# Performance work log

Measured on AMD Instinct MI355X. Metric: run time of the kernel, lower is better.

Reference implementation:

```python
import jax, jax.numpy as jnp
import numpy as np

B, S, D, H = 2, 2048, 1024, 16
HD = D // H                      # head_dim = 64
F_POLY = HD + HD * HD            # 4160 degree-2 poly feature dim
M_HID = 2 * D                    # memory_expansion = 2
FFN_H = int(D * 4 * 2 / 3)       # 2730 SwiGLU hidden
GG_H = 64                        # gamma-gate hidden dim
EPS = 1e-6
OMEGA_W, OMEGA_DECAY = 64, 0.95
TTL_ALPHA, TTL_ETA, NS_ITERS = 0.999, 0.01, 5


def rmsnorm(x, w):
    return x * jax.lax.rsqrt(jnp.mean(x * x, -1, keepdims=True) + EPS) * w


def apply_rope(q, k):
    half = HD // 2
    inv = 1.0 / (10000.0 ** (jnp.arange(half, dtype=jnp.float32) / half))
    fr = jnp.arange(S, dtype=jnp.float32)[:, None] * inv[None, :]  # (S, half)
    cos, sin = jnp.cos(fr), jnp.sin(fr)
    def rot(x):
        x1, x2 = x[..., :half], x[..., half:]
        return jnp.concatenate([x1 * cos - x2 * sin, x1 * sin + x2 * cos], -1)
    return rot(q), rot(k)


def phi2(z):
    # degree-2 polynomial features: [z, vec(z z^T)/sqrt(d)]  -> capacity O(d_k^2)
    outer = (z[..., :, None] * z[..., None, :]).reshape(*z.shape[:-1], HD * HD)
    return jnp.concatenate([z, outer / jnp.sqrt(jnp.float32(HD))], -1)


def memory_forward(x, wk, w1, w2):
    feat = phi2(x @ wk)                     # (B,S,F_POLY)
    return jax.nn.silu(feat @ w1) @ w2      # (B,S,D)


def newton_schulz(G):
    # Muon-style quintic Newton-Schulz orthogonalization
    a, b, c = 3.4445, -4.7750, 2.0315
    X = G / (jnp.linalg.norm(G) + 1e-7)
    tall = X.shape[0] > X.shape[1]
    X = X.T if tall else X
    for _ in range(NS_ITERS):
        A = X @ X.T
        X = a * X + (b * A + c * (A @ A)) @ X
    return X.T if tall else X


def block_forward(x, norm1_w, norm2_w, qkv_w, q_norm_w, k_norm_w,
                  gamma_w1, gamma_w2, mem_wk, mem_w1, mem_w2,
                  memory_gate, wo_w, ffn_w1, ffn_w2, ffn_w3):
    h = rmsnorm(x, norm1_w)
    q, k, v = jnp.split(h @ qkv_w, 3, axis=-1)
    heads = lambda t: t.reshape(B, S, H, HD).transpose(0, 2, 1, 3)  # (B,H,S,HD)
    q, k, v = heads(q), heads(k), heads(v)
    q = rmsnorm(q, q_norm_w)   # qk-norm per head
    k = rmsnorm(k, k_norm_w)
    q, k = apply_rope(q, k)

    # input-dependent gamma gate (B,S,1)
    gamma = jax.nn.sigmoid(jax.nn.silu(h @ gamma_w1) @ gamma_w2)

    # causal QK memory projection: gamma-blended causal mean of keys
    k_cummean = jnp.cumsum(k, axis=2) / jnp.arange(1, S + 1, dtype=k.dtype)[None, None, :, None]
    g = gamma[:, None, :, :]                          # (B,1,S,1)
    q_mem = g * q + (1.0 - g) * k_cummean             # (B,H,S,HD)
    q_mem_flat = q_mem.transpose(0, 2, 1, 3).reshape(B, S, D)
    v_flat = v.transpose(0, 2, 1, 3).reshape(B, S, D)

    # --- TTL: Omega-rule loss + Newton-Schulz update of memory params ---
    pos = jnp.arange(S)
    dpow = jnp.float32(OMEGA_DECAY) ** (S - 1 - pos).astype(jnp.float32)
    dpow = jnp.where(pos >= S - OMEGA_W, dpow, 0.0)   # context-window pruning
    w_omega = gamma[..., 0] * dpow                    # (B,S)

    def omega_loss(wk, w1, w2):
        pred = memory_forward(q_mem_flat, wk, w1, w2)
        per_tok = jnp.sum((pred - v_flat) ** 2, -1)   # (B,S)
        return jnp.sum(w_omega * per_tok) / (jnp.sum(w_omega) + 1e-8)

    gk, g1, g2 = jax.grad(omega_loss, argnums=(0, 1, 2))(mem_wk, mem_w1, mem_w2)
    # momentum S_t = theta*0 + grad (fresh state), update M = alpha*M - eta*NS(S_t)
    mem_wk_u = TTL_ALPHA * mem_wk - TTL_ETA * newton_schulz(gk)
    mem_w1_u = TTL_ALPHA * mem_w1 - TTL_ETA * newton_schulz(g1)
    mem_w2_u = TTL_ALPHA * mem_w2 - TTL_ETA * newton_schulz(g2)

    # --- SWA branch (full causal attention) ---
    attn = jnp.einsum('bhsd,bhtd->bhst', q, k) * (HD ** -0.5)
    causal = jnp.tril(jnp.ones((S, S), dtype=bool))
    attn = jnp.where(causal, attn, -jnp.inf)
    attn = jax.nn.softmax(attn, -1)
    attn_out = jnp.einsum('bhst,bhtd->bhsd', attn, v)
    attn_out = attn_out.transpose(0, 2, 1, 3).reshape(B, S, D) @ wo_w

    # --- memory branch with learned output-level gate ---
    mem_out = memory_forward(q_mem_flat, mem_wk_u, mem_w1_u, mem_w2_u)
    mem_out = jax.nn.sigmoid(memory_gate) * mem_out

    x = x + attn_out + mem_out
    h2 = rmsnorm(x, norm2_w)
    x = x + (jax.nn.silu(h2 @ ffn_w1) * (h2 @ ffn_w3)) @ ffn_w2
    return x


def setup_inputs() -> dict:
    key = jax.random.key(0)
    ks = jax.random.split(key, 16)
    std = 0.02
    return {
        'x': jax.random.normal(ks[0], (B, S, D), jnp.float32),
        'norm1_w': jnp.ones((D,), jnp.float32),
        'norm2_w': jnp.ones((D,), jnp.float32),
        'qkv_w': jax.random.normal(ks[1], (D, 3 * D), jnp.float32) * std,
        'q_norm_w': jnp.ones((HD,), jnp.float32),
        'k_norm_w': jnp.ones((HD,), jnp.float32),
        'gamma_w1': jax.random.normal(ks[2], (D, GG_H), jnp.float32) * std,
        'gamma_w2': jnp.zeros((GG_H, 1), jnp.float32),  # zero-init -> gamma ~ 0.5
        'mem_wk': jax.random.normal(ks[3], (D, HD), jnp.float32) * std,
        'mem_w1': jax.random.normal(ks[4], (F_POLY, M_HID), jnp.float32) * std,
        'mem_w2': jax.random.normal(ks[5], (M_HID, D), jnp.float32) * std,
        'memory_gate': jnp.zeros((1,), jnp.float32),    # layer 0 -> pre-sigmoid 0.0
        'wo_w': jax.random.normal(ks[6], (D, D), jnp.float32) * (std / 2 ** 0.5),
        'ffn_w1': jax.random.normal(ks[7], (D, FFN_H), jnp.float32) * std,
        'ffn_w2': jax.random.normal(ks[8], (FFN_H, D), jnp.float32) * std,
        'ffn_w3': jax.random.normal(ks[9], (D, FFN_H), jnp.float32) * std,
    }


def reference(x, norm1_w, norm2_w, qkv_w, q_norm_w, k_norm_w, gamma_w1, gamma_w2,
              mem_wk, mem_w1, mem_w2, memory_gate, wo_w, ffn_w1, ffn_w2, ffn_w3):
    return block_forward(x, norm1_w, norm2_w, qkv_w, q_norm_w, k_norm_w,
                         gamma_w1, gamma_w2, mem_wk, mem_w1, mem_w2,
                         memory_gate, wo_w, ffn_w1, ffn_w2, ffn_w3)
```

## Files before the change

### kernel.cpp

```cpp
#include <hip/hip_runtime.h>
#include <math.h>

#define Bc 2
#define Sc 2048
#define Dc 1024
#define Hc 16
#define HDc 64
#define FPOLY 4160
#define MHID 2048
#define FFNH 2730
#define FFNHP 2752
#define GGH 64
#define NTOK 4096
#define NACT 128

typedef __bf16 bf16;
typedef __attribute__((ext_vector_type(8))) __bf16 bf16x8;
typedef __attribute__((ext_vector_type(4))) float f32x4;

#define AS1 __attribute__((address_space(1)))
#define AS3 __attribute__((address_space(3)))

__device__ __forceinline__ void gload16(const void* g, void* l) {
    __builtin_amdgcn_global_load_lds((AS1 const void*)g, (AS3 void*)l, 16, 0, 0);
// ... 493 lines not shown
__global__ __launch_bounds__(256) void ns_fused(
    const bf16* __restrict__ Sg, const bf16* __restrict__ Cg,
    bf16* __restrict__ Fcg, bf16* __restrict__ FcTg)
{
    __shared__ bf16 Cl[16384], Ml[16384], MTl[16384], FTl[16384];
    const int z = blockIdx.x;
    const bf16* S = Sg + (size_t)z * 16384;
    bf16* Fc = Fcg + (size_t)z * 16384;
    bf16* FcT = FcTg + (size_t)z * 16384;
    const int tid = threadIdx.x, w = tid >> 6, lane = tid & 63;
    const int lrow = lane & 15, quad = lane >> 4;
    const int bm = w * 32;
    for (int i = tid; i < 2048; i += 256) {
        const int row = i >> 4, c = i & 15;
        *(bf16x8*)&Cl[row * 128 + ((c ^ (row & 7)) << 3)] =
            *(const bf16x8*)(Cg + (size_t)z * 16384 + (size_t)row * 128 + c * 8);
    }
    __syncthreads();
    const int r0 = bm + lrow, r1 = r0 + 16;
    const int rx = lrow & 7;
    f32x4 acc[2][8];
    auto zacc = [&]() {
#pragma unroll
        for (int mt = 0; mt < 2; ++mt)
#pragma unroll
            for (int nt = 0; nt < 8; ++nt) { acc[mt][nt][0] = 0.f; acc[mt][nt][1] = 0.f; acc[mt][nt][2] = 0.f; acc[mt][nt][3] = 0.f; }
    };
    auto inner = [&](bf16x8 af0, bf16x8 af1, const bf16* Bt, int c) {
#pragma unroll
        for (int nt = 0; nt < 8; ++nt) {
            const int br = nt * 16 + lrow;
            bf16x8 bfr = *(const bf16x8*)&Bt[br * 128 + ((c ^ (br & 7)) << 3)];
            acc[0][nt] = __builtin_amdgcn_mfma_f32_16x16x32_bf16(af0, bfr, acc[0][nt], 0, 0, 0);
            acc[1][nt] = __builtin_amdgcn_mfma_f32_16x16x32_bf16(af1, bfr, acc[1][nt], 0, 0, 0);
        }
    };
    auto gemm_ll = [&](const bf16* Al, const bf16* Bt) {
        zacc();
#pragma unroll
        for (int k0 = 0; k0 < 128; k0 += 32) {
            const int c = (k0 >> 3) + quad;
            bf16x8 af0 = *(const bf16x8*)&Al[r0 * 128 + ((c ^ rx) << 3)];
            bf16x8 af1 = *(const bf16x8*)&Al[r1 * 128 + ((c ^ rx) << 3)];
            inner(af0, af1, Bt, c);
        }
    };
    auto gemm_gl = [&](const bf16* Ag, const bf16* Bt) {
        zacc();
#pragma unroll
        for (int k0 = 0; k0 < 128; k0 += 32) {
            const int c = (k0 >> 3) + quad;
            bf16x8 af0 = *(const bf16x8*)(Ag + (size_t)r0 * 128 + k0 + quad * 8);
            bf16x8 af1 = *(const bf16x8*)(Ag + (size_t)r1 * 128 + k0 + quad * 8);
            inner(af0, af1, Bt, c);
        }
    };

    for (int t = 0; t < 5; ++t) {
        gemm_gl(S, Cl);
#pragma unroll
        for (int mt = 0; mt < 2; ++mt)
#pragma unroll
            for (int nt = 0; nt < 8; ++nt)
#pragma unroll
                for (int r = 0; r < 4; ++r) {
                    const int row = bm + mt * 16 + quad * 4 + r, col = nt * 16 + lrow;
                    const bf16 v = (bf16)acc[mt][nt][r];
                    Ml[swz(row, col)] = v;
                    MTl[swz(col, row)] = v;
                }
        __syncthreads();
        gemm_ll(Ml, MTl);
#pragma unroll
        for (int mt = 0; mt < 2; ++mt)
#pragma unroll
            for (int nt = 0; nt < 8; ++nt)
#pragma unroll
                for (int r = 0; r < 4; ++r) {
                    const int row = bm + mt * 16 + quad * 4 + r, col = nt * 16 + lrow;
                    float v = 2.0315f * acc[mt][nt][r] - 4.775f * (float)Ml[swz(row, col)];
                    if (row == col) v += 3.4445f;
                    FTl[swz(col, row)] = (bf16)v;
                    if (t == 0) Fc[(size_t)row * 128 + col] = (bf16)v;
                }
        __syncthreads();
        if (t > 0) {
            gemm_gl(Fc, FTl);
            if (t == 4) {
#pragma unroll
                for (int mt = 0; mt < 2; ++mt)
#pragma unroll
                    for (int nt = 0; nt < 8; ++nt)
#pragma unroll
                        for (int r = 0; r < 4; ++r) {
                            const int row = bm + mt * 16 + quad * 4 + r, col = nt * 16 + lrow;
                            FcT[(size_t)col * 128 + row] = (bf16)acc[mt][nt][r];
                        }
                return;
            }
#pragma unroll
            for (int mt = 0; mt < 2; ++mt)
#pragma unroll
                for (int nt = 0; nt < 8; ++nt)
#pragma unroll
                    for (int r = 0; r < 4; ++r) {
                        const int row = bm + mt * 16 + quad * 4 + r, col = nt * 16 + lrow;
                        Fc[(size_t)row * 128 + col] = (bf16)acc[mt][nt][r];
                    }
        }
        gemm_ll(Cl, FTl);
#pragma unroll
        for (int mt = 0; mt < 2; ++mt)
#pragma unroll
            for (int nt = 0; nt < 8; ++nt)
#pragma unroll
                for (int r = 0; r < 4; ++r) {
                    const int row = bm + mt * 16 + quad * 4 + r, col = nt * 16 + lrow;
                    Ml[swz(col, row)] = (bf16)acc[mt][nt][r];
                }
        __syncthreads();
        gemm_ll(Ml, FTl);
#pragma unroll
        for (int mt = 0; mt < 2; ++mt)
#pragma unroll
            for (int nt = 0; nt < 8; ++nt)
#pragma unroll
                for (int r = 0; r < 4; ++r) {
                    const int row = bm + mt * 16 + quad * 4 + r, col = nt * 16 + lrow;
                    Cl[swz(row, col)] = (bf16)acc[mt][nt][r];
                }
        __syncthreads();
    }
}

__global__ __launch_bounds__(256) void tconv_kernel(
    const float* __restrict__ W, bf16* __restrict__ Wt, int K, int N, int Kpad,
    bf16* __restrict__ Wc)
{
    __shared__ float t[32][33];
    const int k0 = blockIdx.x * 32, n0 = blockIdx.y * 32;
    const int tx = threadIdx.x & 31, ty = threadIdx.x >> 5;
#pragma unroll
    for (int r = 0; r < 4; ++r) {
        int gk = k0 + ty + r * 8, gn = n0 + tx;
        bool ok = (gk < K && gn < N);
        float v = ok ? W[(size_t)gk * N + gn] : 0.f;
        t[ty + r * 8][tx] = v;
        if (Wc && ok) Wc[(size_t)gk * N + gn] = (bf16)v;
    }
    __syncthreads();
#pragma unroll
    for (int r = 0; r < 4; ++r) {
        int gn = n0 + ty + r * 8, gk = k0 + tx;
        if (gn < N && gk < Kpad) Wt[(size_t)gn * Kpad + gk] = (bf16)t[tx][ty + r * 8];
    }
}

__global__ __launch_bounds__(256) void tconv6_kernel(
    const float* __restrict__ s0, const float* __restrict__ s1,
    const float* __restrict__ s2, const float* __restrict__ s3,
    const float* __restrict__ s4, const float* __restrict__ s5,
    bf16* __restrict__ d0, bf16* __restrict__ d1, bf16* __restrict__ d2,
    bf16* __restrict__ d3, bf16* __restrict__ d4, bf16* __restrict__ d5)
{
    const int zz = blockIdx.z;
    const float* W; bf16* Wt; int N;
    if      (zz == 0) { W = s0; Wt = d0; N = 2048; }
    else if (zz == 1) { W = s1; Wt = d1; N = 1024; }
    else if (zz == 2) { W = s2; Wt = d2; N = 64;   }
    else if (zz == 3) { W = s3; Wt = d3; N = 1024; }
    else if (zz == 4) { W = s4; Wt = d4; N = 4160; }
    else              { W = s5; Wt = d5; N = 2048; }
    const int k0 = blockIdx.x * 32, n0 = blockIdx.y * 32;
    if (n0 >= N) return;
    __shared__ float t[32][33];
    const int tx = threadIdx.x & 31, ty = threadIdx.x >> 5;
#pragma unroll
    for (int r = 0; r < 4; ++r) {
        int gk = k0 + ty + r * 8, gn = n0 + tx;
        t[ty + r * 8][tx] = (gk < 128 && gn < N) ? W[(size_t)gk * N + gn] : 0.f;
    }
    __syncthreads();
#pragma unroll
    for (int r = 0; r < 4; ++r) {
        int gn = n0 + ty + r * 8, gk = k0 + tx;
        if (gn < N) Wt[(size_t)gn * 128 + gk] = (bf16)t[tx][ty + r * 8];
    }
}

__global__ __launch_bounds__(256) void vtrans_kernel(
    const bf16* __restrict__ qkv, bf16* __restrict__ vt)
{
    __shared__ bf16 t[32][33];
    const int s0 = blockIdx.x * 32, d0 = blockIdx.y * 32, bh = blockIdx.z;
    const int b = bh >> 4, h = bh & 15;
    const int tx = threadIdx.x & 31, ty = threadIdx.x >> 5;
#pragma unroll
    for (int r = 0; r < 4; ++r) {
        int s = s0 + ty + r * 8;
        t[ty + r * 8][tx] = qkv[((size_t)b * Sc + s) * 3072 + 2048 + h * 64 + d0 + tx];
    }
    __syncthreads();
#pragma unroll
    for (int r = 0; r < 4; ++r) {
        int d = d0 + ty + r * 8;
        vt[((size_t)bh * 64 + d) * Sc + s0 + tx] = t[tx][ty + r * 8];
    }
}

__global__ __launch_bounds__(256) void rms_rows(
    const float* __restrict__ in, const float* __restrict__ w,
    bf16* __restrict__ out, int D)
{
    const int row = blockIdx.x;
    const float* r = in + (size_t)row * D;
    bf16* o = out + (size_t)row * D;
    float s = 0.f;
    for (int i = threadIdx.x; i < D; i += 256) { float v = r[i]; s += v * v; }
    __shared__ float red[256];
    red[threadIdx.x] = s;
    __syncthreads();
    for (int st = 128; st; st >>= 1) {
        if (threadIdx.x < st) red[threadIdx.x] += red[threadIdx.x + st];
        __syncthreads();
    }
    float rs = rsqrtf(red[0] / (float)D + 1e-6f);
    for (int i = threadIdx.x; i < D; i += 256) o[i] = (bf16)(r[i] * rs * w[i]);
}

__global__ __launch_bounds__(256) void gamma_kernel(
    const float* __restrict__ gg1, const float* __restrict__ w2,
    float* __restrict__ gamma)
{
    const int tid = threadIdx.x, w = tid >> 6, lane = tid & 63;
    const int t = blockIdx.x * 4 + w;
    float v = gg1[(size_t)t * GGH + lane];
    v = v / (1.f + expf(-v));
    v *= w2[lane];
#pragma unroll
    for (int off = 32; off; off >>= 1) v += __shfl_xor(v, off);
    if (lane == 0) gamma[t] = 1.f / (1.f + expf(-v));
}

__global__ __launch_bounds__(256) void snr_qk(
    const bf16* __restrict__ src, const float* __restrict__ qw, const float* __restrict__ kw,
    bf16* __restrict__ qd, bf16* __restrict__ kd)
{
    const int tid = threadIdx.x, wv = tid >> 6, lane = tid & 63;
    const int s = blockIdx.x * 4 + wv;
    const int y = blockIdx.y, b = blockIdx.z;
    const int h = y & 15, which = y >> 4;
    const float* w = which ? kw : qw;
    bf16* dst = which ? kd : qd;
    const size_t row = ((size_t)b * Sc + s) * 3072 + which * 1024 + h * 64;
    float v = (float)src[row + lane];
    float ss = v * v;
#pragma unroll
    for (int off = 32; off; off >>= 1) ss += __shfl_xor(ss, off);
    v = v * rsqrtf(ss / 64.f + 1e-6f) * w[lane];
    const int j = lane & 31;
    float inv = powf(10000.f, -(float)j / 32.f);
    float ang = (float)s * inv;
    float sn = sinf(ang), cs = cosf(ang);
    float p = __shfl_xor(v, 32);
    float o;
    if (lane < 32) o = v * cs - p * sn;
    else           o = p * sn + v * cs;
    const size_t od = (((size_t)b * Hc + h) * Sc + s) * 64 + lane;
    dst[od] = (bf16)o;
}

__global__ void kpsum_kernel(const bf16* __restrict__ kn, float* __restrict__ psum)
{
    const int bh = blockIdx.x, c = blockIdx.y, d = threadIdx.x;
    const size_t base = (size_t)bh * Sc * 64 + (size_t)c * 128 * 64 + d;
    float s = 0.f;
    for (int i = 0; i < 128; ++i) s += (float)kn[base + (size_t)i * 64];
    psum[((size_t)bh * 16 + c) * 64 + d] = s;
}

__global__ void qmem2_kernel(
    const bf16* __restrict__ qn, const bf16* __restrict__ kn,
    const float* __restrict__ gamma, const float* __restrict__ psum,
    float* __restrict__ qmem, bf16* __restrict__ qmemb)
{
    const int bh = blockIdx.x, c = blockIdx.y;
    const int b = bh >> 4, hh = bh & 15;
    const int d = threadIdx.x;
    const size_t base = (size_t)bh * Sc * 64;
    float run = 0.f;
    for (int cc = 0; cc < c; ++cc) run += psum[((size_t)bh * 16 + cc) * 64 + d];
    for (int s = c * 128; s < c * 128 + 128; ++s) {
        run += (float)kn[base + (size_t)s * 64 + d];
        float cm = run / (float)(s + 1);
        float g = gamma[b * Sc + s];
        float qv = (float)qn[base + (size_t)s * 64 + d];
        float val = g * qv + (1.f - g) * cm;
        const size_t o = ((size_t)(b * Sc + s)) * Dc + hh * 64 + d;
        qmem[o] = val;
        qmemb[o] = (bf16)val;
    }
}

__global__ __launch_bounds__(256, 4) void attn_mfma(
    const bf16* __restrict__ qn, const bf16* __restrict__ kn,
    const bf16* __restrict__ vt, bf16* __restrict__ outp)
{
    const int flat = blockIdx.x;
    const int glow = flat & 7, t2 = flat >> 3;
    const int xq = t2 & 31, ghigh = t2 >> 5;
    const int g = glow | (ghigh << 3);
    const int h = g & 15, b = g >> 4;
    const int bh = b * Hc + h;
    const int tid = threadIdx.x, w = tid >> 6, lane = tid & 63;
    const int lrow = lane & 15, quad = lane >> 4;
    const int rhalf = w & 1, pgrp = w >> 1;
    __shared__ bf16 Ps[4][16][136];
    __shared__ float Ob[2][16][68];
    __shared__ float Lb[2][16];
    const bf16* kbase = kn + (size_t)bh * Sc * 64;
    const bf16* vtb = vt + (size_t)bh * 64 * Sc;
    const float SC = 0.1803368801f;
#pragma unroll 1
    for (int ti = 0; ti < 2; ++ti) {
        const int zt = ti ? (63 - xq) : xq;
        const int qb = zt * 32;
        const int nc = (qb >> 7) + 1;
        const int par = pgrp ^ ti;
        const int rowg = qb + rhalf * 16 + quad * 4;
        bf16x8 qf[2];
        const bf16* qbase = qn + ((size_t)bh * Sc + qb + rhalf * 16) * 64;
#pragma unroll
        for (int ks = 0; ks < 2; ++ks)
            qf[ks] = *(const bf16x8*)(qbase + (size_t)lrow * 64 + ks * 32 + quad * 8);
        f32x4 oacc[4];
#pragma unroll
        for (int nt = 0; nt < 4; ++nt) { oacc[nt][0] = 0.f; oacc[nt][1] = 0.f; oacc[nt][2] = 0.f; oacc[nt][3] = 0.f; }
        float lsum[4] = {0.f, 0.f, 0.f, 0.f};
        for (int ci = par; ci < nc; ci += 2) {
            const int k0 = ci << 7;
            f32x4 sacc[8];
#pragma unroll
            for (int nt = 0; nt < 8; ++nt) { sacc[nt][0] = 0.f; sacc[nt][1] = 0.f; sacc[nt][2] = 0.f; sacc[nt][3] = 0.f; }
            __builtin_amdgcn_s_setprio(1);
#pragma unroll
            for (int ks = 0; ks < 2; ++ks) {
#pragma unroll
                for (int nh = 0; nh < 2; ++nh) {
                    bf16x8 kf[4];
#pragma unroll
                    for (int j = 0; j < 4; ++j)
                        kf[j] = *(const bf16x8*)(kbase + (size_t)(k0 + (nh * 4 + j) * 16 + lrow) * 64 + ks * 32 + quad * 8);
#pragma unroll
                    for (int j = 0; j < 4; ++j)
                        sacc[nh * 4 + j] = __builtin_amdgcn_mfma_f32_16x16x32_bf16(qf[ks], kf[j], sacc[nh * 4 + j], 0, 0, 0);
                }
            }
            __builtin_amdgcn_s_setprio(0);
#pragma unroll
            for (int nt = 0; nt < 8; ++nt) {
                const int kc = k0 + nt * 16 + lrow;
#pragma unroll
                for (int r = 0; r < 4; ++r) {
                    float p = (kc > rowg + r) ? 0.f : fexp2(fmaf(sacc[nt][r], SC, -12.f));
                    sacc[nt][r] = p;
                    lsum[r] += p;
                }
            }
#pragma unroll
            for (int nt = 0; nt < 8; ++nt)
#pragma unroll
                for (int r = 0; r < 4; ++r)
                    Ps[w][quad * 4 + r][nt * 16 + lrow] = (bf16)sacc[nt][r];
            __builtin_amdgcn_s_setprio(1);
#pragma unroll
            for (int ks2 = 0; ks2 < 4; ++ks2) {
                bf16x8 pf = *(const bf16x8*)&Ps[w][lrow][ks2 * 32 + quad * 8];
#pragma unroll
                for (int nt = 0; nt < 4; ++nt) {
                    bf16x8 vf = *(const bf16x8*)(vtb + (size_t)(nt * 16 + lrow) * Sc + k0 + ks2 * 32 + quad * 8);
                    oacc[nt] = __builtin_amdgcn_mfma_f32_16x16x32_bf16(pf, vf, oacc[nt], 0, 0, 0);
                }
            }
            __builtin_amdgcn_s_setprio(0);
        }
#pragma unroll
        for (int r = 0; r < 4; ++r)
#pragma unroll
            for (int off = 1; off < 16; off <<= 1) lsum[r] += __shfl_xor(lsum[r], off);
        if (pgrp == 1) {
#pragma unroll
            for (int nt = 0; nt < 4; ++nt)
#pragma unroll
                for (int r = 0; r < 4; ++r)
                    Ob[rhalf][quad * 4 + r][nt * 16 + lrow] = oacc[nt][r];
            if (lrow == 0)
#pragma unroll
                for (int r = 0; r < 4; ++r) Lb[rhalf][quad * 4 + r] = lsum[r];
        }
        __syncthreads();
        if (pgrp == 0) {
            float linv[4];
#pragma unroll
            for (int r = 0; r < 4; ++r)
                linv[r] = 1.f / (lsum[r] + Lb[rhalf][quad * 4 + r]);
#pragma unroll
            for (int nt = 0; nt < 4; ++nt)
#pragma unroll
                for (int r = 0; r < 4; ++r) {
                    const float o2 = Ob[rhalf][quad * 4 + r][nt * 16 + lrow];
                    outp[((size_t)b * Sc + rowg + r) * Dc + h * 64 + nt * 16 + lrow] =
                        (bf16)((oacc[nt][r] + o2) * linv[r]);
                }
        }
        __syncthreads();
    }
}

__global__ __launch_bounds__(256) void gather_active(
    const float* __restrict__ qmem, const bf16* __restrict__ qkv,
    float* __restrict__ xa, bf16* __restrict__ xab, float* __restrict__ va)
{
    const int t = blockIdx.x;
    const int b = t >> 6;
    const int s = Sc - 64 + (t & 63);
    const float* qrow = qmem + ((size_t)(b * Sc + s)) * Dc;
    const bf16* vrow = qkv + ((size_t)(b * Sc + s)) * 3072 + 2048;
    for (int i = threadIdx.x; i < Dc; i += 256) {
        float q = qrow[i];
        xa[(size_t)t * Dc + i] = q;
        xab[(size_t)t * Dc + i] = (bf16)q;
        va[(size_t)t * Dc + i] = (float)vrow[i];
    }
}

__global__ void wvec_kernel(const float* __restrict__ gamma,
                            float* __restrict__ wvec, float* __restrict__ wsum)
{
    const int t = threadIdx.x;
    const int b = t >> 6, si = t & 63;
    const int s = Sc - 64 + si;
    float v = gamma[b * Sc + s] * powf(0.95f, (float)(Sc - 1 - s));
    wvec[t] = v;
    __shared__ float red[128];
    red[t] = v; __syncthreads();
    for (int st = 64; st; st >>= 1) { if (t < st) red[t] += red[t + st]; __syncthreads(); }
    if (t == 0) wsum[0] = red[0];
}

__global__ __launch_bounds__(256) void phi2_f32(
    const float* __restrict__ z, float* __restrict__ feat, bf16* __restrict__ featb)
{
    const int f = blockIdx.x * 256 + threadIdx.x;
    const int t = blockIdx.y;
    if (f >= FPOLY) return;
    const float* zr = z + (size_t)t * 64;
    float v;
    if (f < 64) v = zr[f];
    else { int i = (f - 64) >> 6, j = (f - 64) & 63; v = zr[i] * zr[j] * 0.125f; }
    feat[(size_t)t * FPOLY + f] = v;
    featb[(size_t)t * FPOLY + f] = (bf16)v;
}

__global__ __launch_bounds__(256) void phi2_bf16(
    const float* __restrict__ z, bf16* __restrict__ feat)
{
    const int f = blockIdx.x * 256 + threadIdx.x;
    const int t = blockIdx.y;
    if (f >= FPOLY) return;
    const float* zr = z + (size_t)t * 64;
    float v;
    if (f < 64) v = zr[f];
    else { int i = (f - 64) >> 6, j = (f - 64) & 63; v = zr[i] * zr[j] * 0.125f; }
    feat[(size_t)t * FPOLY + f] = (bf16)v;
}

__global__ void dz_kernel(const float* __restrict__ dfeat, const float* __restrict__ za,
                          float* __restrict__ dz, bf16* __restrict__ dzb)
{
    const int t = blockIdx.x;
    const int k = threadIdx.x;
    const float* df = dfeat + (size_t)t * FPOLY;
    const float* z = za + (size_t)t * 64;
    float s1 = 0.f, s2 = 0.f;
    for (int j = 0; j < 64; ++j) {
        float zj = z[j];
        s1 += df[64 + k * 64 + j] * zj;
        s2 += df[64 + j * 64 + k] * zj;
    }
    float v = df[k] + 0.125f * (s1 + s2);
    dz[(size_t)t * 64 + k] = v;
    dzb[(size_t)t * 64 + k] = (bf16)v;
}

__global__ void sgate_kernel(const float* __restrict__ mg, float* __restrict__ out)
{
    out[0] = 1.f / (1.f + expf(-mg[0]));
}

__global__ void swiglu_pack(const bf16* __restrict__ u, bf16* __restrict__ o)
{
    int i = blockIdx.x * 256 + threadIdx.x;
    if (i >= NTOK * FFNHP) return;
    int t = i / FFNHP, k = i % FFNHP;
    if (k >= FFNH) { o[i] = (bf16)0.f; return; }
    float a = (float)u[(size_t)t * 5504 + k];
    float b = (float)u[(size_t)t * 5504 + 2752 + k];
    o[i] = (bf16)(a / (1.f + __expf(-a)) * b);
}

extern "C" void kernel_launch(void* const* d_in, const int* in_sizes, int n_in,
                              void* d_out, int out_size, void* d_ws, size_t ws_size,
                              hipStream_t stream)
{
    const float* x     = (const float*)d_in[0];
    const float* n1w   = (const float*)d_in[1];
    const float* n2w   = (const float*)d_in[2];
    const float* qkvw  = (const float*)d_in[3];
    const float* qnw   = (const float*)d_in[4];
    const float* knw   = (const float*)d_in[5];
    const float* gw1   = (const float*)d_in[6];
    const float* gw2   = (const float*)d_in[7];
    const float* mwk   = (const float*)d_in[8];
    const float* mw1   = (const float*)d_in[9];
    const float* mw2   = (const float*)d_in[10];
    const float* mgate = (const float*)d_in[11];
    const float* wow   = (const float*)d_in[12];
    const float* fw1   = (const float*)d_in[13];
    const float* fw2   = (const float*)d_in[14];
    const float* fw3   = (const float*)d_in[15];
    float* outp = (float*)d_out;

    char* base = (char*)d_ws;
    size_t off = 0;
    auto takeB = [&](size_t bytes) { char* p = base + off; off += (bytes + 255) & ~(size_t)255; return p; };

    char* slabA  = takeB(22544384);
    char* slabE  = takeB(22544384);
    char* slabBC = takeB(16777216);
    char* slabD  = takeB(8388608);
    char* slabF  = takeB(8388608);
    char* slabG  = takeB(17301504);
    float* partA = (float*)slabA;
    bf16* vt     = (bf16*)slabA;
    bf16* featC4 = (bf16*)slabA;
    bf16* ff13b  = (bf16*)slabA;
    float* qmem  = (float*)slabE;
    bf16* qnb = (bf16*)slabBC;    bf16* knb = (bf16*)(slabBC + 8388608);
    float* x2 = (float*)slabBC;
    bf16* qmemb = (bf16*)slabD;
    bf16* t1b4  = (bf16*)slabD;
    bf16* attnb = (bf16*)slabF;
    bf16* hb = (bf16*)slabG;      bf16* mw1b = (bf16*)slabG;
    bf16* w1uT = (bf16*)slabG;    bf16* h2b = (bf16*)slabG;
    bf16* qkvb = (bf16*)takeB(25165824);
    bf16* ffpk = qkvb;

    bf16* qkvwT = (bf16*)takeB(6291456);
    bf16* gw1T  = (bf16*)takeB(262144);
    bf16* wowT  = (bf16*)takeB(2097152);
    bf16* mw1T  = (bf16*)takeB(17039360);
    bf16* mw2T  = (bf16*)takeB(4194304);
    bf16* fw13T = (bf16*)takeB(11272192);
    bf16* fw2T  = (bf16*)takeB(5636096);
    bf16* mw2b  = (bf16*)takeB(4194304);
    bf16* mwkTb = (bf16*)takeB(262144);
    bf16* wkuTb = (bf16*)takeB(262144);
    bf16* w2uT  = (bf16*)takeB(4194304);

    float* zf    = (float*)takeB(1048576);
    float* gg1   = (float*)takeB(1048576);
    float* gamma = (float*)takeB(16384);
    float* wvec  = (float*)takeB(512);
    float* scal  = (float*)takeB(256);
    float* psum  = (float*)takeB(131072);
    float* xa    = (float*)takeB(524288);
    float* va    = (float*)takeB(524288);
    float* za    = (float*)takeB(32768);
    float* featA = (float*)takeB(2129920);
    float* ua    = (float*)takeB(1048576);
    float* sua   = (float*)takeB(1048576);
    float* dpreda= (float*)takeB(524288);
    float* dua   = (float*)takeB(1048576);
    float* dfeata= (float*)takeB(2129920);
    float* dza   = (float*)takeB(32768);
    float* SA    = (float*)takeB(196608);
    float* CA    = (float*)takeB(196608);
    bf16* featAb = (bf16*)takeB(1064960);
    bf16* suab   = (bf16*)takeB(524288);
    bf16* xab    = (bf16*)takeB(262144);
    bf16* duab   = (bf16*)takeB(524288);
    bf16* dpredab= (bf16*)takeB(262144);
    bf16* dzab   = (bf16*)takeB(16384);
    bf16* PT1Tb  = (bf16*)takeB(524288);
    bf16* PT2Tb  = (bf16*)takeB(262144);
    bf16* PT3Tb  = (bf16*)takeB(32768);
    bf16* duaTb  = (bf16*)takeB(524288);
    bf16* dpredaTb=(bf16*)takeB(262144);
    bf16* dzaTb  = (bf16*)takeB(32768);
    bf16* xaTb   = (bf16*)takeB(262144);
    bf16* featATb= (bf16*)takeB(1081344);
    bf16* suaTb  = (bf16*)takeB(524288);
    bf16* Sb16  = (bf16*)takeB(98304);
    bf16* Cb16  = (bf16*)takeB(98304);
    bf16* FcAb  = (bf16*)takeB(98304);
    bf16* FcTAb = (bf16*)takeB(98304);

    auto gemmB = [&](int outbf, int cinbf, const bf16* A, const bf16* Bt,
                     const void* Cin, void* C, int M, int N, int K, int ldc,
                     float alpha, float beta, int act, const float* sptr) {
        dim3 grid((N + 127) / 128, M / 128);
        if (outbf && cinbf) gemm_bt<1, 1><<<grid, 256, 0, stream>>>(A, Bt, Cin, C, M, N, K, ldc, alpha, beta, act, sptr);
        else if (outbf)     gemm_bt<1, 0><<<grid, 256, 0, stream>>>(A, Bt, Cin, C, M, N, K, ldc, alpha, beta, act, sptr);
        else                gemm_bt<0, 0><<<grid, 256, 0, stream>>>(A, Bt, Cin, C, M, N, K, ldc, alpha, beta, act, sptr);
    };
    auto gemm64 = [&](const bf16* A, const bf16* Bt, const float* Cin, float* C,
                      int M, int N, int K, int ldc, const float* sptr) {
        dim3 grid(N / 64, M / 128);
        gemm_bt64<<<grid, 256, 0, stream>>>(A, Bt, Cin, C, M, N, K, ldc, sptr);
    };
    auto gdir = [&](int outbf, int cinbf, const bf16* A, const bf16* Bt,
                    const void* Cin, void* C, int M, int N, int K, int ldc,
                    float alpha, float beta, int act, const float* sptr) {
        dim3 grid((N + 127) / 128, (M + 127) / 128);
        if (outbf && cinbf)      gemm_direct<1, 1><<<grid, 256, 0, stream>>>(A, Bt, Cin, C, M, N, K, ldc, alpha, beta, act, sptr);
        else if (outbf)          gemm_direct<1, 0><<<grid, 256, 0, stream>>>(A, Bt, Cin, C, M, N, K, ldc, alpha, beta, act, sptr);
        else if (cinbf)          gemm_direct<0, 1><<<grid, 256, 0, stream>>>(A, Bt, Cin, C, M, N, K, ldc, alpha, beta, act, sptr);
        else                     gemm_direct<0, 0><<<grid, 256, 0, stream>>>(A, Bt, Cin, C, M, N, K, ldc, alpha, beta, act, sptr);
    };
    auto skp = [&](const bf16* A, const bf16* Bt, float* out,
                   int M, int N, int K, int KC) {
        int SK = (K + KC - 1) / KC;
        gemm_skp<<<dim3((N + 127) / 128, (M + 127) / 128, SK), 256, 0, stream>>>(A, Bt, partA, M, N, K, KC);
        int MN = M * N;
        skred<<<(MN + 255) / 256, 256, 0, stream>>>(partA, out, SK, MN);
    };
    auto tconv = [&](const float* W, bf16* Wt, int K, int N, int Kpad, bf16* Wc) {
        tconv_kernel<<<dim3((Kpad + 31) / 32, (N + 31) / 32), 256, 0, stream>>>(W, Wt, K, N, Kpad, Wc);
    };

    tconv(qkvw, qkvwT, Dc, 3 * Dc, Dc, nullptr);
    tconv(gw1, gw1T, Dc, GGH, Dc, nullptr);
    tconv(wow, wowT, Dc, Dc, Dc, nullptr);
    tconv(mw2, mw2T, MHID, Dc, MHID, mw2b);
    tconv(fw1, fw13T, Dc, FFNH, Dc, nullptr);
    tconv(fw3, fw13T + (size_t)2752 * Dc, Dc, FFNH, Dc, nullptr);
    tconv(fw2, fw2T, FFNH, Dc, FFNHP, nullptr);
    tconv(mwk, mwkTb, Dc, HDc, Dc, nullptr);
    sgate_kernel<<<1, 1, 0, stream>>>(mgate, scal + 2);

    rms_rows<<<NTOK, 256, 0, stream>>>(x, n1w, hb, Dc);
    gemmB(1, 0, hb, qkvwT, nullptr, qkvb, NTOK, 3 * Dc, Dc, 3 * Dc, 1.f, 0.f, 0, nullptr);
    snr_qk<<<dim3(Sc / 4, 32, Bc), 256, 0, stream>>>(qkvb, qnw, knw, qnb, knb);
    skp(hb, gw1T, gg1, NTOK, GGH, Dc, 256);
    gamma_kernel<<<NTOK / 4, 256, 0, stream>>>(gg1, gw2, gamma);
    tconv(mw1, mw1T, FPOLY, MHID, FPOLY, mw1b);

    vtrans_kernel<<<dim3(Sc / 32, 2, Bc * Hc), 256, 0, stream>>>(qkvb, vt);
    kpsum_kernel<<<dim3(Bc * Hc, 16), 64, 0, stream>>>(knb, psum);
    qmem2_kernel<<<dim3(Bc * Hc, 16), 64, 0, stream>>>(qnb, knb, gamma, psum, qmem, qmemb);
    attn_mfma<<<dim3(1024), 256, 0, stream>>>(qnb, knb, vt, attnb);

    gather_active<<<NACT, 256, 0, stream>>>(qmem, qkvb, xa, xab, va);
    wvec_kernel<<<1, 128, 0, stream>>>(gamma, wvec, scal);

    skp(xab, mwkTb, za, NACT, HDc, Dc, 64);
    phi2_f32<<<dim3((FPOLY + 255) / 256, NACT), 256, 0, stream>>>(za, featA, featAb);
    gemm_skp<<<dim3(16, 1, 15), 256, 0, stream>>>(featAb, mw1T, partA, NACT, MHID, FPOLY, 288);
    skred_silu<<<1024, 256, 0, stream>>>(partA, ua, sua, suab);
    gemm_skp<<<dim3(8, 1, 16), 256, 0, stream>>>(suab, mw2T, partA, NACT, Dc, MHID, 128);
    skred_dpred<<<512, 256, 0, stream>>>(partA, va, wvec, scal, dpreda, dpredab);
    gemm_skp<<<dim3(16, 1, 8), 256, 0, stream>>>(dpredab, mw2b, partA, NACT, MHID, Dc, 128);
    skred_dsilu<<<1024, 256, 0, stream>>>(partA, ua, dua, duab);
    skp(duab, mw1b, dfeata, NACT, FPOLY, MHID, 256);
    dz_kernel<<<NACT, 64, 0, stream>>>(dfeata, za, dza, dzab);

    tconv6_kernel<<<dim3(4, 130, 6), 256, 0, stream>>>(
        dua, dpreda, dza, xa, featA, sua,
        duaTb, dpredaTb, dzaTb, xaTb, featATb, suaTb);

    gram_trick<<<1, 256, 0, stream>>>(za, SA);
    gram_bat<<<dim3(32, 5), 256, 0, stream>>>(suab, xab, duab, dpredab, dzab, partA);
    gram_red<<<320, 256, 0, stream>>>(partA, SA, CA);
    ns_norm_kernel<<<3, 256, 0, stream>>>(SA, CA, Sb16, Cb16, scal + 8);
    ns_fused<<<3, 256, 0, stream>>>(Sb16, Cb16, FcAb, FcTAb);
    gdir3_kernel<<<dim3(1, 16, 3), 256, 0, stream>>>(
        duaTb, dpredaTb, dzaTb, FcTAb, PT1Tb, PT2Tb, PT3Tb, scal + 8);

    gdir(1, 1, PT3Tb, xaTb, mwkTb, wkuTb, HDc, Dc, 128, Dc, -0.01f, 0.999f, 0, nullptr);
    gemmB(1, 1, PT1Tb, featATb, mw1T, w1uT, MHID, FPOLY, 128, FPOLY, -0.01f, 0.999f, 0, nullptr);
    gemmB(1, 1, PT2Tb, suaTb, mw2T, w2uT, Dc, MHID, 128, MHID, -0.01f, 0.999f, 0, nullptr);

    gemm64(attnb, wowT, x, x2, NTOK, Dc, Dc, Dc, nullptr);
    skp(qmemb, wkuTb, zf, NTOK, HDc, Dc, 128);

    phi2_bf16<<<dim3((FPOLY + 255) / 256, NTOK), 256, 0, stream>>>(zf, featC4);
    gemmB(1, 0, featC4, w1uT, nullptr, t1b4, NTOK, MHID, FPOLY, MHID, 1.f, 0.f, 1, nullptr);
    gemm64(t1b4, w2uT, x2, x2, NTOK, Dc, MHID, Dc, scal + 2);

    rms_rows<<<NTOK, 256, 0, stream>>>(x2, n2w, h2b, Dc);
    gemmB(1, 0, h2b, fw13T, nullptr, ff13b, NTOK, 5482, Dc, 5504, 1.f, 0.f, 0, nullptr);
    swiglu_pack<<<(NTOK * FFNHP + 255) / 256, 256, 0, stream>>>(ff13b, ffpk);
    gemm64(ffpk, fw2T, x2, outp, NTOK, Dc, FFNHP, Dc, nullptr);
}
```

Baseline: 1.162 ms.

## Stage K/V tiles in double-buffered LDS and widen attention query tiles

The causal attention kernel now stages each 128-key K and V^T tile into XOR-swizzled shared memory with async global-to-LDS loads. The tiles are double-buffered so the next tile loads while the current one is computed. Each block handles two 64-row query tiles, paired for causal balance, and every wave owns 16 rows over the full key range, which removes the cross-wave partial-sum merge. The grid is halved and the occupancy hint is dropped, so there is less parallelism and higher LDS use per block in exchange for removing redundant global K/V reads by each wave.

```diff
diff --git a/kernel.cpp b/kernel.cpp
--- a/kernel.cpp
+++ b/kernel.cpp
@@ -819,119 +819,140 @@
     }
 }
 
-__global__ __launch_bounds__(256, 4) void attn_mfma(
+__global__ __launch_bounds__(256) void attn_mfma(
     const bf16* __restrict__ qn, const bf16* __restrict__ kn,
     const bf16* __restrict__ vt, bf16* __restrict__ outp)
 {
     const int flat = blockIdx.x;
     const int glow = flat & 7, t2 = flat >> 3;
-    const int xq = t2 & 31, ghigh = t2 >> 5;
+    const int p = t2 & 15, ghigh = t2 >> 4;
     const int g = glow | (ghigh << 3);
     const int h = g & 15, b = g >> 4;
     const int bh = b * Hc + h;
     const int tid = threadIdx.x, w = tid >> 6, lane = tid & 63;
     const int lrow = lane & 15, quad = lane >> 4;
-    const int rhalf = w & 1, pgrp = w >> 1;
-    __shared__ bf16 Ps[4][16][136];
-    __shared__ float Ob[2][16][68];
-    __shared__ float Lb[2][16];
+    __shared__ bf16 Ks[2][128 * 64];
+    __shared__ bf16 Vs[2][64 * 128];
+    __shared__ bf16 Ps[4][16][72];
     const bf16* kbase = kn + (size_t)bh * Sc * 64;
     const bf16* vtb = vt + (size_t)bh * 64 * Sc;
     const float SC = 0.1803368801f;
-#pragma unroll 1
-    for (int ti = 0; ti < 2; ++ti) {
-        const int zt = ti ? (63 - xq) : xq;
-        const int qb = zt * 32;
-        const int nc = (qb >> 7) + 1;
-        const int par = pgrp ^ ti;
-        const int rowg = qb + rhalf * 16 + quad * 4;
-        bf16x8 qf[2];
-        const bf16* qbase = qn + ((size_t)bh * Sc + qb + rhalf * 16) * 64;
+    const int zt0 = p, zt1 = 31 - p;
+    const int nc0 = (zt0 >> 1) + 1, nc1 = (zt1 >> 1) + 1;
+    const int nct = nc0 + nc1;
+    const int krr = lane >> 3, kur = lane & 7;
+    const int vrr = lane >> 4, vur = lane & 15;
+    auto stage = [&](int bi, int k0) {
+#pragma unroll
+        for (int rr = 0; rr < 4; ++rr) {
+            const int row = (rr * 4 + w) * 8 + krr;
+            gload16(kbase + (size_t)(k0 + row) * 64 + ((kur ^ krr) << 3),
+                    (char*)&Ks[bi][0] + (rr * 4 + w) * 1024);
+        }
+#pragma unroll
+        for (int rr = 0; rr < 4; ++rr) {
+            const int vrow = (rr * 4 + w) * 4 + vrr;
+            gload16(vtb + (size_t)vrow * Sc + k0 + ((vur ^ (vrow & 7)) << 3),
+                    (char*)&Vs[bi][0] + (rr * 4 + w) * 1024);
+        }
+    };
+    int qb = zt0 * 64;
+    int rowg = qb + w * 16 + quad * 4;
+    bf16x8 qf[2];
+    {
+        const bf16* qbase = qn + ((size_t)bh * Sc + qb + w * 16) * 64;
 #pragma unroll
         for (int ks = 0; ks < 2; ++ks)
             qf[ks] = *(const bf16x8*)(qbase + (size_t)lrow * 64 + ks * 32 + quad * 8);
-        f32x4 oacc[4];
-#pragma unroll
-        for (int nt = 0; nt < 4; ++nt) { oacc[nt][0] = 0.f; oacc[nt][1] = 0.f; oacc[nt][2] = 0.f; oacc[nt][3] = 0.f; }
-        float lsum[4] = {0.f, 0.f, 0.f, 0.f};
-        for (int ci = par; ci < nc; ci += 2) {
-            const int k0 = ci << 7;
-            f32x4 sacc[8];
-#pragma unroll
-            for (int nt = 0; nt < 8; ++nt) { sacc[nt][0] = 0.f; sacc[nt][1] = 0.f; sacc[nt][2] = 0.f; sacc[nt][3] = 0.f; }
+    }
+    f32x4 oacc[4];
+#pragma unroll
+    for (int nt = 0; nt < 4; ++nt) { oacc[nt][0] = 0.f; oacc[nt][1] = 0.f; oacc[nt][2] = 0.f; oacc[nt][3] = 0.f; }
+    float lsum[4] = {0.f, 0.f, 0.f, 0.f};
+    auto writeout = [&]() {
+#pragma unroll
+        for (int r = 0; r < 4; ++r)
+#pragma unroll
+            for (int off = 1; off < 16; off <<= 1) lsum[r] += __shfl_xor(lsum[r], off);
+        float linv[4];
+#pragma unroll
+        for (int r = 0; r < 4; ++r) linv[r] = 1.f / lsum[r];
+#pragma unroll
+        for (int nt = 0; nt < 4; ++nt)
+#pragma unroll
+            for (int r = 0; r < 4; ++r)
+                outp[((size_t)b * Sc + rowg + r) * Dc + h * 64 + nt * 16 + lrow] =
+                    (bf16)(oacc[nt][r] * linv[r]);
+    };
+    int buf = 0;
+    stage(0, 0);
+    __syncthreads();
+    for (int it = 0; it < nct; ++it) {
+        const int nxt = it + 1;
+        if (nxt < nct)
+            stage(buf ^ 1, (nxt < nc0 ? nxt : nxt - nc0) * 128);
+        const int k0 = (it < nc0 ? it : it - nc0) * 128;
+        f32x4 sacc[8];
+#pragma unroll
+        for (int nt = 0; nt < 8; ++nt) { sacc[nt][0] = 0.f; sacc[nt][1] = 0.f; sacc[nt][2] = 0.f; sacc[nt][3] = 0.f; }
+        __builtin_amdgcn_s_setprio(1);
+#pragma unroll
+        for (int ks = 0; ks < 2; ++ks)
+#pragma unroll
+            for (int nt = 0; nt < 8; ++nt) {
+                const int krow = nt * 16 + lrow;
+                bf16x8 kf = *(const bf16x8*)&Ks[buf][krow * 64 + (((ks * 4 + quad) ^ (lrow & 7)) << 3)];
+                sacc[nt] = __builtin_amdgcn_mfma_f32_16x16x32_bf16(qf[ks], kf, sacc[nt], 0, 0, 0);
+            }
+        __builtin_amdgcn_s_setprio(0);
+#pragma unroll
+        for (int nt = 0; nt < 8; ++nt) {
+            const int kc = k0 + nt * 16 + lrow;
+#pragma unroll
+            for (int r = 0; r < 4; ++r) {
+                float pv = (kc > rowg + r) ? 0.f : fexp2(fmaf(sacc[nt][r], SC, -12.f));
+                sacc[nt][r] = pv;
+                lsum[r] += pv;
+            }
+        }
+#pragma unroll
+        for (int half = 0; half < 2; ++half) {
+#pragma unroll
+            for (int nt = 0; nt < 4; ++nt)
+#pragma unroll
+                for (int r = 0; r < 4; ++r)
+                    Ps[w][quad * 4 + r][nt * 16 + lrow] = (bf16)sacc[half * 4 + nt][r];
             __builtin_amdgcn_s_setprio(1);
 #pragma unroll
-            for (int ks = 0; ks < 2; ++ks) {
-#pragma unroll
-                for (int nh = 0; nh < 2; ++nh) {
-                    bf16x8 kf[4];
-#pragma unroll
-                    for (int j = 0; j < 4; ++j)
-                        kf[j] = *(const bf16x8*)(kbase + (size_t)(k0 + (nh * 4 + j) * 16 + lrow) * 64 + ks * 32 + quad * 8);
-#pragma unroll
-                    for (int j = 0; j < 4; ++j)
-                        sacc[nh * 4 + j] = __builtin_amdgcn_mfma_f32_16x16x32_bf16(qf[ks], kf[j], sacc[nh * 4 + j], 0, 0, 0);
-                }
-            }
-            __builtin_amdgcn_s_setprio(0);
-#pragma unroll
-            for (int nt = 0; nt < 8; ++nt) {
-                const int kc = k0 + nt * 16 + lrow;
-#pragma unroll
-                for (int r = 0; r < 4; ++r) {
-                    float p = (kc > rowg + r) ? 0.f : fexp2(fmaf(sacc[nt][r], SC, -12.f));
-                    sacc[nt][r] = p;
-                    lsum[r] += p;
-                }
-            }
-#pragma unroll
-            for (int nt = 0; nt < 8; ++nt)
-#pragma unroll
-                for (int r = 0; r < 4; ++r)
-                    Ps[w][quad * 4 + r][nt * 16 + lrow] = (bf16)sacc[nt][r];
-            __builtin_amdgcn_s_setprio(1);
-#pragma unroll
-            for (int ks2 = 0; ks2 < 4; ++ks2) {
-                bf16x8 pf = *(const bf16x8*)&Ps[w][lrow][ks2 * 32 + quad * 8];
+            for (int k2 = 0; k2 < 2; ++k2) {
+                const int ks2 = half * 2 + k2;
+                bf16x8 pf = *(const bf16x8*)&Ps[w][lrow][k2 * 32 + quad * 8];
 #pragma unroll
                 for (int nt = 0; nt < 4; ++nt) {
-                    bf16x8 vf = *(const bf16x8*)(vtb + (size_t)(nt * 16 + lrow) * Sc + k0 + ks2 * 32 + quad * 8);
+                    const int vrow = nt * 16 + lrow;
+                    bf16x8 vf = *(const bf16x8*)&Vs[buf][vrow * 128 + (((ks2 * 4 + quad) ^ (lrow & 7)) << 3)];
                     oacc[nt] = __builtin_amdgcn_mfma_f32_16x16x32_bf16(pf, vf, oacc[nt], 0, 0, 0);
                 }
             }
             __builtin_amdgcn_s_setprio(0);
         }
-#pragma unroll
-        for (int r = 0; r < 4; ++r)
-#pragma unroll
-            for (int off = 1; off < 16; off <<= 1) lsum[r] += __shfl_xor(lsum[r], off);
-        if (pgrp == 1) {
-#pragma unroll
-            for (int nt = 0; nt < 4; ++nt)
-#pragma unroll
-                for (int r = 0; r < 4; ++r)
-                    Ob[rhalf][quad * 4 + r][nt * 16 + lrow] = oacc[nt][r];
-            if (lrow == 0)
-#pragma unroll
-                for (int r = 0; r < 4; ++r) Lb[rhalf][quad * 4 + r] = lsum[r];
-        }
         __syncthreads();
-        if (pgrp == 0) {
-            float linv[4];
-#pragma unroll
-            for (int r = 0; r < 4; ++r)
-                linv[r] = 1.f / (lsum[r] + Lb[rhalf][quad * 4 + r]);
-#pragma unroll
-            for (int nt = 0; nt < 4; ++nt)
-#pragma unroll
-                for (int r = 0; r < 4; ++r) {
-                    const float o2 = Ob[rhalf][quad * 4 + r][nt * 16 + lrow];
-                    outp[((size_t)b * Sc + rowg + r) * Dc + h * 64 + nt * 16 + lrow] =
-                        (bf16)((oacc[nt][r] + o2) * linv[r]);
-                }
-        }
-        __syncthreads();
-    }
+        buf ^= 1;
+        if (it == nc0 - 1) {
+            writeout();
+            qb = zt1 * 64;
+            rowg = qb + w * 16 + quad * 4;
+            const bf16* qbase = qn + ((size_t)bh * Sc + qb + w * 16) * 64;
+#pragma unroll
+            for (int ks = 0; ks < 2; ++ks)
+                qf[ks] = *(const bf16x8*)(qbase + (size_t)lrow * 64 + ks * 32 + quad * 8);
+#pragma unroll
+            for (int nt = 0; nt < 4; ++nt) { oacc[nt][0] = 0.f; oacc[nt][1] = 0.f; oacc[nt][2] = 0.f; oacc[nt][3] = 0.f; }
+#pragma unroll
+            for (int r = 0; r < 4; ++r) lsum[r] = 0.f;
+        }
+    }
+    writeout();
 }
 
 __global__ __launch_bounds__(256) void gather_active(
@@ -1176,7 +1197,7 @@
     vtrans_kernel<<<dim3(Sc / 32, 2, Bc * Hc), 256, 0, stream>>>(qkvb, vt);
     kpsum_kernel<<<dim3(Bc * Hc, 16), 64, 0, stream>>>(knb, psum);
     qmem2_kernel<<<dim3(Bc * Hc, 16), 64, 0, stream>>>(qnb, knb, gamma, psum, qmem, qmemb);
-    attn_mfma<<<dim3(1024), 256, 0, stream>>>(qnb, knb, vt, attnb);
+    attn_mfma<<<dim3(512), 256, 0, stream>>>(qnb, knb, vt, attnb);
 
     gather_active<<<NACT, 256, 0, stream>>>(qmem, qkvb, xa, xab, va);
     wvec_kernel<<<1, 128, 0, stream>>>(gamma, wvec, scal);
```

Result: faster. 1.072 ms (-7.8%).
